# Kernel optimization log

Measured on AMD Instinct MI355X. Metric: run time of the kernel, lower is better.

The kernel has to match this reference:

```python
import jax, jax.numpy as jnp
import numpy as np

D_MODEL = 1024
D_INTERNAL = 256


def setup_inputs() -> dict:
    key = jax.random.key(0)
    ks = jax.random.split(key, 10)
    s = lambda fan_in: 1.0 / np.sqrt(fan_in)
    inp = {
        "input_vecs": jax.random.normal(ks[0], (4, 2048, D_MODEL), dtype=jnp.float32),
        # Linear weights stored as (in, out) for x @ W
        "wq": jax.random.uniform(ks[1], (D_MODEL, D_INTERNAL), minval=-s(D_MODEL), maxval=s(D_MODEL), dtype=jnp.float32),
        "wk": jax.random.uniform(ks[2], (D_MODEL, D_INTERNAL), minval=-s(D_MODEL), maxval=s(D_MODEL), dtype=jnp.float32),
        "wv": jax.random.uniform(ks[3], (D_MODEL, D_MODEL), minval=-s(D_MODEL), maxval=s(D_MODEL), dtype=jnp.float32),
        "wo": jax.random.uniform(ks[4], (D_MODEL, D_MODEL), minval=-s(D_MODEL), maxval=s(D_MODEL), dtype=jnp.float32),
        "bo": jax.random.uniform(ks[5], (D_MODEL,), minval=-s(D_MODEL), maxval=s(D_MODEL), dtype=jnp.float32),
        "w1": jax.random.uniform(ks[6], (D_MODEL, D_INTERNAL), minval=-s(D_MODEL), maxval=s(D_MODEL), dtype=jnp.float32),
        "b1": jax.random.uniform(ks[7], (D_INTERNAL,), minval=-s(D_MODEL), maxval=s(D_MODEL), dtype=jnp.float32),
        "w2": jax.random.uniform(ks[8], (D_INTERNAL, D_MODEL), minval=-s(D_INTERNAL), maxval=s(D_INTERNAL), dtype=jnp.float32),
        "b2": jax.random.uniform(ks[9], (D_MODEL,), minval=-s(D_INTERNAL), maxval=s(D_INTERNAL), dtype=jnp.float32),
    }
    return inp


def reference(input_vecs, wq, wk, wv, wo, bo, w1, b1, w2, b2):
    # Single-head self-attention (causal=False default path)
    q = jnp.einsum("btd,dk->btk", input_vecs, wq)  # (B,T,d_internal)
    k = jnp.einsum("btd,dk->btk", input_vecs, wk)
    v = jnp.einsum("btd,de->bte", input_vecs, wv)  # (B,T,d_model)
    scale = 1.0 / jnp.sqrt(jnp.asarray(q.shape[-1], dtype=q.dtype))
    scores = jnp.einsum("bqk,btk->bqt", q, k) * scale  # (B,T,T)
    attn = jax.nn.softmax(scores, axis=-1)
    context = jnp.einsum("bqt,bte->bqe", attn, v)  # (B,T,d_model)
    context = jnp.einsum("bte,eo->bto", context, wo) + bo
    residual = input_vecs + context
    h = jax.nn.relu(jnp.einsum("btd,dk->btk", residual, w1) + b1)
    ff = jnp.einsum("btk,kd->btd", h, w2) + b2
    out = residual + ff
    return out, attn
```

## Files before the change

### kernel.cpp

```cpp
#include <hip/hip_runtime.h>

typedef unsigned short u16;
typedef unsigned int u32;
typedef __bf16 bf16x8 __attribute__((ext_vector_type(8)));
typedef float f32x4 __attribute__((ext_vector_type(4)));

#define MTOT 8192
#define DM 1024
#define DI 256
#define TT 2048

__device__ __forceinline__ u16 f2bf(float f) {
    u32 u = __float_as_uint(f);
    return (u16)((u + 0x7fffu + ((u >> 16) & 1u)) >> 16);
}
__device__ __forceinline__ float b2f(u16 b) {
    return __uint_as_float((u32)b << 16);
}

__device__ __forceinline__ void transpose_tile(const float* __restrict__ in,
                                               u16* __restrict__ out, int K, int N,
                                               int bx, int by) {
    __shared__ float t[32][33];
    int n0 = bx * 32, k0 = by * 32;
    int tx = threadIdx.x & 31, ty = threadIdx.x >> 5;
    #pragma unroll
    for (int i = ty; i < 32; i += 8) t[i][tx] = in[(long)(k0 + i) * N + n0 + tx];
    __syncthreads();
    #pragma unroll
    for (int i = ty; i < 32; i += 8) out[(long)(n0 + i) * K + k0 + tx] = f2bf(t[tx][i]);
}

__global__ __launch_bounds__(256) void prep_kernel(
    const float* __restrict__ x, u16* __restrict__ Xb,
    const float* __restrict__ wq, const float* __restrict__ wk, u16* __restrict__ Wqk_t,
    const float* __restrict__ wv, u16* __restrict__ Wv_t,
    const float* __restrict__ wo, u16* __restrict__ Wo_t,
    const float* __restrict__ w1, u16* __restrict__ W1_t,
    const float* __restrict__ w2, u16* __restrict__ W2_t)
{
    int b = blockIdx.x;
    if (b < 1024) {
        long n4 = (long)MTOT * DM / 4;
        long i = (long)b * 256 + threadIdx.x;
        long stride = 1024L * 256;
        for (; i < n4; i += stride) {
            float4 v = reinterpret_cast<const float4*>(x)[i];
            union { u16 u[4]; uint2 p; } o;
            o.u[0] = f2bf(v.x); o.u[1] = f2bf(v.y); o.u[2] = f2bf(v.z); o.u[3] = f2bf(v.w);
            reinterpret_cast<uint2*>(Xb)[i] = o.p;
        }
        return;
    }
    b -= 1024;
    if (b < 256)        { transpose_tile(wq, Wqk_t,              1024,  256, b & 7,  b >> 3); return; }
    b -= 256;
    if (b < 256)        { transpose_tile(wk, Wqk_t + 256 * 1024, 1024,  256, b & 7,  b >> 3); return; }
    b -= 256;
    if (b < 1024)       { transpose_tile(wv, Wv_t,               1024, 1024, b & 31, b >> 5); return; }
    b -= 1024;
    if (b < 1024)       { transpose_tile(wo, Wo_t,               1024, 1024, b & 31, b >> 5); return; }
    b -= 1024;
    if (b < 256)        { transpose_tile(w1, W1_t,               1024,  256, b & 7,  b >> 3); return; }
    b -= 256;
    transpose_tile(w2, W2_t, 256, 1024, b & 31, b >> 5);
}

__global__ __launch_bounds__(256) void softmax_kernel(u16* __restrict__ Sb, float* __restrict__ attn) {
    long row = blockIdx.x;
    int tid = threadIdx.x;
    uint4 q = reinterpret_cast<uint4*>(Sb + row * (long)TT)[tid];
    u32 w4[4] = {q.x, q.y, q.z, q.w};
    float vv[8];
    #pragma unroll
    for (int j = 0; j < 4; ++j) {
        vv[2 * j]     = __uint_as_float(w4[j] << 16);
        vv[2 * j + 1] = __uint_as_float(w4[j] & 0xffff0000u);
    }
    float m = vv[0];
    #pragma unroll
    for (int j = 1; j < 8; ++j) m = fmaxf(m, vv[j]);
    #pragma unroll
    for (int off = 32; off; off >>= 1) m = fmaxf(m, __shfl_xor(m, off));
    __shared__ float redm[4], reds[4];
    if ((tid & 63) == 0) redm[tid >> 6] = m;
    __syncthreads();
    m = fmaxf(fmaxf(redm[0], redm[1]), fmaxf(redm[2], redm[3]));
    float s = 0.f;
    #pragma unroll
    for (int j = 0; j < 8; ++j) { vv[j] = __expf(vv[j] - m); s += vv[j]; }
    #pragma unroll
    for (int off = 32; off; off >>= 1) s += __shfl_xor(s, off);
    if ((tid & 63) == 0) reds[tid >> 6] = s;
    __syncthreads();
    s = reds[0] + reds[1] + reds[2] + reds[3];
    float inv = 1.0f / s;
    #pragma unroll
    for (int j = 0; j < 8; ++j) vv[j] *= inv;
    float* p = attn + row * (long)TT;
    reinterpret_cast<float4*>(p)[tid * 2]     = make_float4(vv[0], vv[1], vv[2], vv[3]);
    reinterpret_cast<float4*>(p)[tid * 2 + 1] = make_float4(vv[4], vv[5], vv[6], vv[7]);
    union { u16 u[8]; uint4 q; } pk;
    #pragma unroll
    for (int j = 0; j < 8; ++j) pk.u[j] = f2bf(vv[j]);
    reinterpret_cast<uint4*>(Sb + row * (long)TT)[tid] = pk.q;
}

template<int MODE>
__device__ __forceinline__ void gemm_body(
    u16* As, u16* Bs,
    const u16* __restrict__ A, int lda,
    const u16* __restrict__ Bt, int ldb,
    u16* __restrict__ Cb, int ldcb,
    float* __restrict__ Cf, int ldcf,
    int K, float scale,
    const float* __restrict__ bias,
    const u16* __restrict__ addend_b, int ld_add,
    long tile_m, long tile_n)
{
    const int tid = threadIdx.x;
    const int w = tid >> 6;
    const int l = tid & 63;
    const int lane15 = l & 15;
    const int lhi = l >> 4;

    const int srow = w * 8 + (l >> 3);
    const int scol = (((l & 7) ^ (l >> 3)) << 4) >> 1;

    const u16* aptr = A + (tile_m + srow) * (long)lda + scol;
    const u16* bptr = Bt + (tile_n + srow) * (long)ldb + scol;

    f32x4 acc[4][4] = {};

    const int wr = (w >> 1) * 64;
    const int wc = (w & 1) * 64;

    for (int k0 = 0; k0 < K; k0 += 64) {
        #pragma unroll
        for (int i = 0; i < 4; ++i) {
            __builtin_amdgcn_global_load_lds(
                (const __attribute__((address_space(1))) void*)(aptr + (long)i * 32 * lda + k0),
                (__attribute__((address_space(3))) void*)((char*)As + i * 4096 + w * 1024),
                16, 0, 0);
        }
        #pragma unroll
        for (int i = 0; i < 4; ++i) {
            __builtin_amdgcn_global_load_lds(
                (const __attribute__((address_space(1))) void*)(bptr + (long)i * 32 * ldb + k0),
                (__attribute__((address_space(3))) void*)((char*)Bs + i * 4096 + w * 1024),
                16, 0, 0);
        }
        __syncthreads();
        #pragma unroll
        for (int kk = 0; kk < 2; ++kk) {
            bf16x8 af[4], bfr[4];
            const int kb = (kk * 32 + lhi * 8) * 2;
            #pragma unroll
            for (int m = 0; m < 4; ++m) {
                int r = wr + m * 16 + lane15;
                af[m] = *reinterpret_cast<const bf16x8*>(
                    (const char*)As + r * 128 + (kb ^ ((r & 7) << 4)));
            }
            #pragma unroll
            for (int n = 0; n < 4; ++n) {
                int r = wc + n * 16 + lane15;
                bfr[n] = *reinterpret_cast<const bf16x8*>(
                    (const char*)Bs + r * 128 + (kb ^ ((r & 7) << 4)));
            }
            #pragma unroll
            for (int m = 0; m < 4; ++m)
                #pragma unroll
                for (int n = 0; n < 4; ++n)
                    acc[m][n] = __builtin_amdgcn_mfma_f32_16x16x32_bf16(
                        af[m], bfr[n], acc[m][n], 0, 0, 0);
        }
        __syncthreads();
    }

    #pragma unroll
    for (int m = 0; m < 4; ++m) {
        #pragma unroll
        for (int n = 0; n < 4; ++n) {
            long grow0 = tile_m + wr + m * 16 + lhi * 4;
            long gcol  = tile_n + wc + n * 16 + lane15;
            #pragma unroll
            for (int r = 0; r < 4; ++r) {
                long grow = grow0 + r;
                float v = acc[m][n][r];
                if (MODE == 0) v *= scale;
                if (MODE == 3 || MODE == 6 || MODE == 7) v += bias[gcol];
                if (MODE == 6 || MODE == 7) v += b2f(addend_b[grow * (long)ld_add + gcol]);
                if (MODE == 3) v = fmaxf(v, 0.0f);
                if (MODE == 0 || MODE == 3 || MODE == 6) Cb[grow * (long)ldcb + gcol] = f2bf(v);
                if (MODE == 1) Cb[gcol * (long)ldcb + grow] = f2bf(v);
                if (MODE == 7) Cf[grow * (long)ldcf + gcol] = v;
            }
        }
    }
}

__device__ __forceinline__ int xcd_swizzle(int bid, int nb) {
    return (bid & 7) * (nb >> 3) + (bid >> 3);
}

template<int MODE>
__global__ __launch_bounds__(256) void gemm_bt(
    const u16* __restrict__ A, long sA, int lda,
    const u16* __restrict__ Bt, long sB, int ldb,
    u16* __restrict__ Cb, long sCb, int ldcb,
    float* __restrict__ Cf, long sCf, int ldcf,
    int K, float scale,
    const float* __restrict__ bias,
    const u16* __restrict__ addend_b, long sAdd, int ld_add,
    int gx, int gy)
{
    __shared__ __attribute__((aligned(16))) u16 As[128 * 64];
    __shared__ __attribute__((aligned(16))) u16 Bs[128 * 64];

    int lid = xcd_swizzle(blockIdx.x, gridDim.x);
    int x = lid % gx;
    int t = lid / gx;
    int y = t % gy;
    int z = t / gy;

    gemm_body<MODE>(As, Bs,
                    A + (long)z * sA, lda, Bt + (long)z * sB, ldb,
                    Cb + (long)z * sCb, ldcb, Cf + (long)z * sCf, ldcf,
                    K, scale, bias,
                    addend_b ? addend_b + (long)z * sAdd : addend_b, ld_add,
                    (long)y * 128, (long)x * 128);
}

__global__ __launch_bounds__(256) void gemm_qkv(
    const u16* __restrict__ Xb, const u16* __restrict__ Wqk_t, u16* __restrict__ QKb,
    const u16* __restrict__ Wv_t, u16* __restrict__ Vt)
{
    __shared__ __attribute__((aligned(16))) u16 As[128 * 64];
    __shared__ __attribute__((aligned(16))) u16 Bs[128 * 64];

    int lid = xcd_swizzle(blockIdx.x, gridDim.x);
    if (lid < 256) {
        int x = lid & 3, y = lid >> 2;
        gemm_body<0>(As, Bs, Xb, 1024, Wqk_t, 1024, QKb, 512,
                     (float*)nullptr, 0, 1024, 1.0f,
                     (const float*)nullptr, (const u16*)nullptr, 0,
                     (long)y * 128, (long)x * 128);
    } else {
        int l2 = lid - 256;
        int x = l2 & 7, y = l2 >> 3;
        gemm_body<1>(As, Bs, Xb, 1024, Wv_t, 1024, Vt, 8192,
                     (float*)nullptr, 0, 1024, 1.0f,
                     (const float*)nullptr, (const u16*)nullptr, 0,
                     (long)y * 128, (long)x * 128);
    }
}

extern "C" void kernel_launch(void* const* d_in, const int* in_sizes, int n_in,
                              void* d_out, int out_size, void* d_ws, size_t ws_size,
                              hipStream_t stream)
{
    const float* x  = (const float*)d_in[0];
    const float* wq = (const float*)d_in[1];
    const float* wk = (const float*)d_in[2];
    const float* wv = (const float*)d_in[3];
    const float* wo = (const float*)d_in[4];
    const float* bo = (const float*)d_in[5];
    const float* w1 = (const float*)d_in[6];
    const float* b1 = (const float*)d_in[7];
    const float* w2 = (const float*)d_in[8];
    const float* b2 = (const float*)d_in[9];

    float* out_f  = (float*)d_out;
    float* attn_f = out_f + (long)MTOT * DM;

    char* ws = (char*)d_ws;
    u16* Xb    = (u16*)(ws + 0);
    u16* Wqk_t = (u16*)(ws + 16777216);
    u16* Wv_t  = (u16*)(ws + 17825792);
    u16* Wo_t  = (u16*)(ws + 19922944);
    u16* W1_t  = (u16*)(ws + 22020096);
    u16* W2_t  = (u16*)(ws + 22544384);
    u16* QKb   = (u16*)(ws + 23068672);
    u16* Vt    = (u16*)(ws + 31457280);
    u16* attnb = (u16*)(ws + 48234496);
    u16* ctxb  = (u16*)(ws + 81788928);
    u16* res_b = (u16*)(ws + 98566144);
    u16* hb    = QKb;

    dim3 blk(256);

    prep_kernel<<<dim3(4096), blk, 0, stream>>>(x, Xb, wq, wk, Wqk_t, wv, Wv_t,
                                                wo, Wo_t, w1, W1_t, w2, W2_t);
    gemm_qkv<<<dim3(768), blk, 0, stream>>>(Xb, Wqk_t, QKb, Wv_t, Vt);
    gemm_bt<0><<<dim3(1024), blk, 0, stream>>>(
        QKb, (long)2048 * 512, 512, QKb + 256, (long)2048 * 512, 512,
        attnb, (long)2048 * 2048, 2048, (float*)nullptr, 0L, 0,
        256, 0.0625f, (const float*)nullptr, (const u16*)nullptr, 0L, 0, 16, 16);
    softmax_kernel<<<dim3(8192), blk, 0, stream>>>(attnb, attn_f);
    gemm_bt<0><<<dim3(512), blk, 0, stream>>>(
        attnb, (long)2048 * 2048, 2048, Vt, 2048L, 8192,
        ctxb, (long)2048 * 1024, 1024, (float*)nullptr, 0L, 0,
        2048, 1.0f, (const float*)nullptr, (const u16*)nullptr, 0L, 0, 8, 16);
    gemm_bt<6><<<dim3(512), blk, 0, stream>>>(
        ctxb, 0L, 1024, Wo_t, 0L, 1024, res_b, 0L, 1024,
        (float*)nullptr, 0L, 0, 1024, 1.0f, bo, Xb, 0L, 1024, 8, 64);
    gemm_bt<3><<<dim3(128), blk, 0, stream>>>(
        res_b, 0L, 1024, W1_t, 0L, 1024, hb, 0L, 256,
        (float*)nullptr, 0L, 0, 1024, 1.0f, b1, (const u16*)nullptr, 0L, 0, 2, 64);
    gemm_bt<7><<<dim3(512), blk, 0, stream>>>(
        hb, 0L, 256, W2_t, 0L, 256, (u16*)nullptr, 0L, 0,
        out_f, 0L, 1024, 256, 1.0f, b2, res_b, 0L, 1024, 8, 64);
}
```

Baseline: 203.8 us.

## Fold Wo into Wv to drop the separate output-projection GEMM

```diff
diff --git a/kernel.cpp b/kernel.cpp
--- a/kernel.cpp
+++ b/kernel.cpp
@@ -31,37 +31,38 @@
     for (int i = ty; i < 32; i += 8) out[(long)(n0 + i) * K + k0 + tx] = f2bf(t[tx][i]);
 }
 
+__device__ __forceinline__ void cvt_range(const float* __restrict__ in,
+                                          u16* __restrict__ out, long n4, int b, int nb) {
+    long i = (long)b * 256 + threadIdx.x;
+    long stride = (long)nb * 256;
+    for (; i < n4; i += stride) {
+        float4 v = reinterpret_cast<const float4*>(in)[i];
+        union { u16 u[4]; uint2 p; } o;
+        o.u[0] = f2bf(v.x); o.u[1] = f2bf(v.y); o.u[2] = f2bf(v.z); o.u[3] = f2bf(v.w);
+        reinterpret_cast<uint2*>(out)[i] = o.p;
+    }
+}
+
 __global__ __launch_bounds__(256) void prep_kernel(
     const float* __restrict__ x, u16* __restrict__ Xb,
     const float* __restrict__ wq, const float* __restrict__ wk, u16* __restrict__ Wqk_t,
-    const float* __restrict__ wv, u16* __restrict__ Wv_t,
+    const float* __restrict__ wv, u16* __restrict__ Wv_b,
     const float* __restrict__ wo, u16* __restrict__ Wo_t,
     const float* __restrict__ w1, u16* __restrict__ W1_t,
     const float* __restrict__ w2, u16* __restrict__ W2_t)
 {
     int b = blockIdx.x;
-    if (b < 1024) {
-        long n4 = (long)MTOT * DM / 4;
-        long i = (long)b * 256 + threadIdx.x;
-        long stride = 1024L * 256;
-        for (; i < n4; i += stride) {
-            float4 v = reinterpret_cast<const float4*>(x)[i];
-            union { u16 u[4]; uint2 p; } o;
-            o.u[0] = f2bf(v.x); o.u[1] = f2bf(v.y); o.u[2] = f2bf(v.z); o.u[3] = f2bf(v.w);
-            reinterpret_cast<uint2*>(Xb)[i] = o.p;
-        }
-        return;
-    }
+    if (b < 1024) { cvt_range(x, Xb, (long)MTOT * DM / 4, b, 1024); return; }
     b -= 1024;
-    if (b < 256)        { transpose_tile(wq, Wqk_t,              1024,  256, b & 7,  b >> 3); return; }
+    if (b < 256)  { transpose_tile(wq, Wqk_t,              1024,  256, b & 7,  b >> 3); return; }
     b -= 256;
-    if (b < 256)        { transpose_tile(wk, Wqk_t + 256 * 1024, 1024,  256, b & 7,  b >> 3); return; }
+    if (b < 256)  { transpose_tile(wk, Wqk_t + 256 * 1024, 1024,  256, b & 7,  b >> 3); return; }
     b -= 256;
-    if (b < 1024)       { transpose_tile(wv, Wv_t,               1024, 1024, b & 31, b >> 5); return; }
+    if (b < 256)  { cvt_range(wv, Wv_b, (long)DM * DM / 4, b, 256); return; }
+    b -= 256;
+    if (b < 1024) { transpose_tile(wo, Wo_t,               1024, 1024, b & 31, b >> 5); return; }
     b -= 1024;
-    if (b < 1024)       { transpose_tile(wo, Wo_t,               1024, 1024, b & 31, b >> 5); return; }
-    b -= 1024;
-    if (b < 256)        { transpose_tile(w1, W1_t,               1024,  256, b & 7,  b >> 3); return; }
+    if (b < 256)  { transpose_tile(w1, W1_t,               1024,  256, b & 7,  b >> 3); return; }
     b -= 256;
     transpose_tile(w2, W2_t, 256, 1024, b & 31, b >> 5);
 }
@@ -233,7 +234,7 @@
 
 __global__ __launch_bounds__(256) void gemm_qkv(
     const u16* __restrict__ Xb, const u16* __restrict__ Wqk_t, u16* __restrict__ QKb,
-    const u16* __restrict__ Wv_t, u16* __restrict__ Vt)
+    const u16* __restrict__ Wvo_t, u16* __restrict__ VWt)
 {
     __shared__ __attribute__((aligned(16))) u16 As[128 * 64];
     __shared__ __attribute__((aligned(16))) u16 Bs[128 * 64];
@@ -248,7 +249,7 @@
     } else {
         int l2 = lid - 256;
         int x = l2 & 7, y = l2 >> 3;
-        gemm_body<1>(As, Bs, Xb, 1024, Wv_t, 1024, Vt, 8192,
+        gemm_body<1>(As, Bs, Xb, 1024, Wvo_t, 1024, VWt, 8192,
                      (float*)nullptr, 0, 1024, 1.0f,
                      (const float*)nullptr, (const u16*)nullptr, 0,
                      (long)y * 128, (long)x * 128);
@@ -276,34 +277,35 @@
     char* ws = (char*)d_ws;
     u16* Xb    = (u16*)(ws + 0);
     u16* Wqk_t = (u16*)(ws + 16777216);
-    u16* Wv_t  = (u16*)(ws + 17825792);
+    u16* Wv_b  = (u16*)(ws + 17825792);
     u16* Wo_t  = (u16*)(ws + 19922944);
     u16* W1_t  = (u16*)(ws + 22020096);
     u16* W2_t  = (u16*)(ws + 22544384);
-    u16* QKb   = (u16*)(ws + 23068672);
-    u16* Vt    = (u16*)(ws + 31457280);
-    u16* attnb = (u16*)(ws + 48234496);
-    u16* ctxb  = (u16*)(ws + 81788928);
-    u16* res_b = (u16*)(ws + 98566144);
+    u16* Wvo_t = (u16*)(ws + 23068672);
+    u16* QKb   = (u16*)(ws + 25165824);
+    u16* VWt   = (u16*)(ws + 33554432);
+    u16* attnb = (u16*)(ws + 50331648);
+    u16* res_b = (u16*)(ws + 83886080);
     u16* hb    = QKb;
 
     dim3 blk(256);
 
-    prep_kernel<<<dim3(4096), blk, 0, stream>>>(x, Xb, wq, wk, Wqk_t, wv, Wv_t,
+    prep_kernel<<<dim3(3328), blk, 0, stream>>>(x, Xb, wq, wk, Wqk_t, wv, Wv_b,
                                                 wo, Wo_t, w1, W1_t, w2, W2_t);
-    gemm_qkv<<<dim3(768), blk, 0, stream>>>(Xb, Wqk_t, QKb, Wv_t, Vt);
+    gemm_bt<1><<<dim3(64), blk, 0, stream>>>(
+        Wv_b, 0L, 1024, Wo_t, 0L, 1024, Wvo_t, 0L, 1024,
+        (float*)nullptr, 0L, 0, 1024, 1.0f, (const float*)nullptr,
+        (const u16*)nullptr, 0L, 0, 8, 8);
+    gemm_qkv<<<dim3(768), blk, 0, stream>>>(Xb, Wqk_t, QKb, Wvo_t, VWt);
     gemm_bt<0><<<dim3(1024), blk, 0, stream>>>(
         QKb, (long)2048 * 512, 512, QKb + 256, (long)2048 * 512, 512,
         attnb, (long)2048 * 2048, 2048, (float*)nullptr, 0L, 0,
         256, 0.0625f, (const float*)nullptr, (const u16*)nullptr, 0L, 0, 16, 16);
     softmax_kernel<<<dim3(8192), blk, 0, stream>>>(attnb, attn_f);
-    gemm_bt<0><<<dim3(512), blk, 0, stream>>>(
-        attnb, (long)2048 * 2048, 2048, Vt, 2048L, 8192,
-        ctxb, (long)2048 * 1024, 1024, (float*)nullptr, 0L, 0,
-        2048, 1.0f, (const float*)nullptr, (const u16*)nullptr, 0L, 0, 8, 16);
     gemm_bt<6><<<dim3(512), blk, 0, stream>>>(
-        ctxb, 0L, 1024, Wo_t, 0L, 1024, res_b, 0L, 1024,
-        (float*)nullptr, 0L, 0, 1024, 1.0f, bo, Xb, 0L, 1024, 8, 64);
+        attnb, (long)2048 * 2048, 2048, VWt, 2048L, 8192,
+        res_b, (long)2048 * 1024, 1024, (float*)nullptr, 0L, 0,
+        2048, 1.0f, bo, Xb, (long)2048 * 1024, 1024, 8, 16);
     gemm_bt<3><<<dim3(128), blk, 0, stream>>>(
         res_b, 0L, 1024, W1_t, 0L, 1024, hb, 0L, 256,
         (float*)nullptr, 0L, 0, 1024, 1.0f, b1, (const u16*)nullptr, 0L, 0, 2, 64);
```

Result: faster. 197.7 us (-3.0%).
